# Kernel tuning notes

Hardware: AMD Instinct MI355X
Metric: run time of the kernel (lower is better)

The kernel has to match this reference:

```python
import jax, jax.numpy as jnp
import numpy as np

SEQ, BATCH, IN = 512, 256, 15
H1, H2, FC_HID, NUM_CLASSES = 512, 512, 64, 1


def setup_inputs() -> dict:
    key = jax.random.key(0)
    ks = jax.random.split(key, 14)
    def u(k, shape, fan_in):
        b = 1.0 / np.sqrt(fan_in)
        return jax.random.uniform(k, shape, jnp.float32, -b, b)
    return {
        "x": jax.random.normal(ks[0], (SEQ, BATCH, IN), jnp.float32),
        # PyTorch LSTM params, gate order i,f,g,o stacked along dim 0
        "W_ih1": u(ks[1], (4 * H1, IN), H1),
        "W_hh1": u(ks[2], (4 * H1, H1), H1),
        "b_ih1": u(ks[3], (4 * H1,), H1),
        "b_hh1": u(ks[4], (4 * H1,), H1),
        "W_ih2": u(ks[5], (4 * H2, H1), H2),
        "W_hh2": u(ks[6], (4 * H2, H2), H2),
        "b_ih2": u(ks[7], (4 * H2,), H2),
        "b_hh2": u(ks[8], (4 * H2,), H2),
        "fc1_w": u(ks[9], (FC_HID, H2), H2),
        "fc1_b": u(ks[10], (FC_HID,), H2),
        "fc_w": u(ks[11], (NUM_CLASSES, FC_HID), FC_HID),
        "fc_b": u(ks[12], (NUM_CLASSES,), FC_HID),
    }


def _lstm_cell(x_t, h, c, W_ih, W_hh, b_ih, b_hh):
    # gates: [B, 4H], PyTorch gate order i, f, g, o
    g = x_t @ W_ih.T + b_ih + h @ W_hh.T + b_hh
    i, f, gg, o = jnp.split(g, 4, axis=-1)
    c_new = jax.nn.sigmoid(f) * c + jax.nn.sigmoid(i) * jnp.tanh(gg)
    h_new = jax.nn.sigmoid(o) * jnp.tanh(c_new)
    return h_new, c_new


def reference(x, W_ih1, W_hh1, b_ih1, b_hh1, W_ih2, W_hh2, b_ih2, b_hh2,
              fc1_w, fc1_b, fc_w, fc_b):
    S, B, _ = x.shape
    init = (jnp.zeros((B, H1), x.dtype), jnp.zeros((B, H1), x.dtype),
            jnp.zeros((B, H2), x.dtype), jnp.zeros((B, H2), x.dtype))

    def step(carry, x_t):
        h1, c1, h2, c2 = carry
        h1, c1 = _lstm_cell(x_t, h1, c1, W_ih1, W_hh1, b_ih1, b_hh1)
        h2, c2 = _lstm_cell(h1, h2, c2, W_ih2, W_hh2, b_ih2, b_hh2)
        return (h1, c1, h2, c2), None

    (h1, c1, h2, c2), _ = jax.lax.scan(step, init, x)
    # MLP head on final-timestep top-layer hidden state; `out += out` doubles it
    hn = jax.nn.relu(h2)
    out = jax.nn.relu(hn @ fc1_w.T + fc1_b)
    out = out @ fc_w.T + fc_b
    return out + out
```

## Files before the change

kernel.cpp:

```cpp
#include <hip/hip_runtime.h>
#include <cstdint>
#include <cstddef>

typedef __attribute__((ext_vector_type(8))) short short8;
typedef __attribute__((ext_vector_type(4))) float floatx4;

constexpr int kSeq = 512;
constexpr int kBatch = 256;
constexpr int kIn = 15;
constexpr int kH = 512;
constexpr int kG = 4 * kH;
constexpr int kRing = 17;
constexpr size_t kHSlot = (size_t)kBatch * kH;
constexpr size_t kShmemBytes = 131072 + 4096;

__device__ __forceinline__ unsigned short f2bf(float f) {
    union { float f; unsigned u; } v; v.f = f;
    unsigned u = v.u;
    return (unsigned short)((u + 0x7fffu + ((u >> 16) & 1u)) >> 16);
}

__device__ __forceinline__ float sigm(float x) { return 1.0f / (1.0f + __expf(-x)); }
__device__ __forceinline__ float tanh_(float x) { return 1.0f - 2.0f / (1.0f + __expf(2.0f * x)); }

#define LLC_STORE16(P, V)                                                     \
    asm volatile("global_store_dwordx4 %0, %1, off sc0 sc1"                   \
                 :: "v"(P), "v"(V) : "memory")

__device__ __forceinline__ void waitf(const int* flags, int tgt, int lane, int& fc) {
    if (tgt <= 0) return;
    bool watch = (lane < 32);
    if (__all(!watch || fc >= tgt)) return;
    for (;;) {
        if (watch && fc < tgt)
            fc = __hip_atomic_load(flags + lane * 16,
                                   __ATOMIC_RELAXED, __HIP_MEMORY_SCOPE_AGENT);
        if (__all(!watch || fc >= tgt)) return;
        __builtin_amdgcn_s_sleep(1);
    }
}

__global__ void k_conv(const float* __restrict__ src, unsigned short* __restrict__ dst, int n) {
    int i = blockIdx.x * blockDim.x + threadIdx.x;
    if (i < n) dst[i] = f2bf(src[i]);
}

__global__ void k_conv_pad(const float* __restrict__ src, unsigned short* __restrict__ dst, int rows) {
    int i = blockIdx.x * blockDim.x + threadIdx.x;
    if (i >= rows * 32) return;
    int r = i >> 5, k = i & 31;
    dst[i] = (k < kIn) ? f2bf(src[r * kIn + k]) : (unsigned short)0;
}

__global__ __launch_bounds__(256) void k_persist(
    const unsigned short* __restrict__ whh1b,
    const unsigned short* __restrict__ wih1b,
    const unsigned short* __restrict__ wih2b,
    const unsigned short* __restrict__ whh2b,
    const unsigned short* __restrict__ xb,
    const float* __restrict__ bih1, const float* __restrict__ bhh1,
    const float* __restrict__ bih2, const float* __restrict__ bhh2,
    unsigned short* __restrict__ h1r,
    unsigned short* __restrict__ h2r,
    float* __restrict__ h2f,
    int* __restrict__ flags)
{
    extern __shared__ unsigned short lw[];
    const int bid = blockIdx.x;
    const int g = bid & 3;
    const int role = bid >> 2;
    const bool is2 = role >= 32;
    const int rid = role & 31;
    const int j0 = rid << 4;
    const int tid = (int)threadIdx.x;
    const int wave = tid >> 6;
    const int lane = tid & 63;
    const int lcol = lane & 15;
    const int quad = lane >> 4;
    const int m0 = (g << 6) + wave * 16;
    const int arow = m0 + lcol;
    const int koff = quad * 8;

    int* f1 = flags + g * 1024;
    int* f2 = f1 + 512;
    int* myflag = (is2 ? f2 : f1) + rid * 16;
    unsigned short* scr = lw + 65536 + wave * 384;

    if (!is2) {
        for (int i = tid; i < 4096; i += 256) {
            int ln = i >> 6, gg = ln >> 4, u = ln & 15;
            int c = i & 63, kk = c >> 2, qd = c & 3;
            *(short8*)&lw[((gg * 16 + kk) << 9) + ((qd * 16 + u) << 3)] =
                *(const short8*)&whh1b[(size_t)((gg << 9) + j0 + u) * kH + c * 8];
        }
        for (int i = tid; i < 256; i += 256) {
            int ln = i >> 2, gg = ln >> 4, u = ln & 15;
            int qd = i & 3;
            *(short8*)&lw[((64 + gg) << 9) + ((qd * 16 + u) << 3)] =
                *(const short8*)&wih1b[((gg << 9) + j0 + u) * 32 + qd * 8];
        }
    } else {
        for (int i = tid; i < 4096; i += 256) {
            int ln = i >> 6, gg = ln >> 4, u = ln & 15;
            int c = i & 63, kk = c >> 2, qd = c & 3;
            int dst = ((gg * 16 + kk) << 9) + ((qd * 16 + u) << 3);
            size_t src = (size_t)((gg << 9) + j0 + u) * kH + c * 8;
            *(short8*)&lw[dst] = *(const short8*)&wih2b[src];
            *(short8*)&lw[dst + (64 << 9)] = *(const short8*)&whh2b[src];
        }
    }
    float bsum[4];
#pragma unroll
    for (int gg = 0; gg < 4; ++gg) {
        int n = (gg << 9) + j0 + lcol;
        bsum[gg] = is2 ? (bih2[n] + bhh2[n]) : (bih1[n] + bhh1[n]);
    }
    __syncthreads();

    float creg[4] = {0.f, 0.f, 0.f, 0.f};
    int fc1 = 0, fc2 = 0;

    if (!is2) {
        for (int s = 0; s < kSeq; ++s) {
            if ((s & 15) == 0) {
                if (wave == 0) { waitf(f1, s, lane, fc1); waitf(f2, s, lane, fc2); }
                __syncthreads();
                __builtin_amdgcn_fence(__ATOMIC_ACQUIRE, "agent");
            }
            floatx4 acc[4];
#pragma unroll
            for (int gg = 0; gg < 4; ++gg)
                acc[gg] = (floatx4){bsum[gg], bsum[gg], bsum[gg], bsum[gg]};

            short8 ax = *(const short8*)(xb + ((size_t)s * kBatch + arow) * 32 + koff);

            if (wave == 0) waitf(f1, s, lane, fc1);
            __syncthreads();

            const unsigned short* hp = h1r + (size_t)((s + 16) % kRing) * kHSlot
                                       + (size_t)arow * kH + koff;
            short8 a[16];
#pragma unroll
            for (int kk = 0; kk < 16; ++kk) a[kk] = *(const short8*)(hp + kk * 32);
#pragma unroll
            for (int kk = 0; kk < 16; ++kk) {
#pragma unroll
                for (int gg = 0; gg < 4; ++gg) {
                    short8 b = *(const short8*)&lw[((gg * 16 + kk) << 9) + (lane << 3)];
                    acc[gg] = __builtin_amdgcn_mfma_f32_16x16x32_bf16(a[kk], b, acc[gg], 0, 0, 0);
                }
            }
#pragma unroll
            for (int gg = 0; gg < 4; ++gg) {
                short8 b = *(const short8*)&lw[((64 + gg) << 9) + (lane << 3)];
                acc[gg] = __builtin_amdgcn_mfma_f32_16x16x32_bf16(ax, b, acc[gg], 0, 0, 0);
            }

            unsigned short* hw = h1r + (size_t)(s % kRing) * kHSlot;
#pragma unroll
            for (int r = 0; r < 4; ++r) {
                int row = quad * 4 + r;
                float gi = acc[0][r], gf = acc[1][r], ggv = acc[2][r], go = acc[3][r];
                float cn = sigm(gf) * creg[r] + sigm(gi) * tanh_(ggv);
                float hn = sigm(go) * tanh_(cn);
                creg[r] = cn;
                scr[row * 24 + lcol] = f2bf(hn);
            }
            __syncthreads();
            if (lane < 32) {
                int row = lane >> 1, seg = lane & 1;
                short8 v = *(short8*)&scr[row * 24 + seg * 8];
                unsigned short* gp = hw + (size_t)(m0 + row) * kH + j0 + seg * 8;
                LLC_STORE16(gp, v);
            }
            __builtin_amdgcn_s_waitcnt(0);
            __syncthreads();
            if (tid == 0)
                __hip_atomic_store(myflag, s + 1,
                                   __ATOMIC_RELAXED, __HIP_MEMORY_SCOPE_AGENT);
        }
    } else {
        for (int u = 0; u < kSeq; ++u) {
            if ((u & 15) == 0) {
                if (wave == 0) { waitf(f1, u, lane, fc1); waitf(f2, u, lane, fc2); }
                __syncthreads();
                __builtin_amdgcn_fence(__ATOMIC_ACQUIRE, "agent");
            }
            floatx4 acc[4];
#pragma unroll
            for (int gg = 0; gg < 4; ++gg)
                acc[gg] = (floatx4){bsum[gg], bsum[gg], bsum[gg], bsum[gg]};

            if (wave == 0) waitf(f2, u, lane, fc2);
            __syncthreads();

            const unsigned short* hp2 = h2r + (size_t)((u + 16) % kRing) * kHSlot
                                        + (size_t)arow * kH + koff;
            short8 a[16];
#pragma unroll
            for (int kk = 0; kk < 16; ++kk) a[kk] = *(const short8*)(hp2 + kk * 32);
#pragma unroll
            for (int kk = 0; kk < 16; ++kk) {
#pragma unroll
                for (int gg = 0; gg < 4; ++gg) {
                    short8 b = *(const short8*)&lw[((64 + gg * 16 + kk) << 9) + (lane << 3)];
                    acc[gg] = __builtin_amdgcn_mfma_f32_16x16x32_bf16(a[kk], b, acc[gg], 0, 0, 0);
                }
            }

            if (wave == 0) waitf(f1, u + 1, lane, fc1);
            __syncthreads();

            const unsigned short* hp1 = h1r + (size_t)(u % kRing) * kHSlot
                                        + (size_t)arow * kH + koff;
#pragma unroll
            for (int kk = 0; kk < 16; ++kk) a[kk] = *(const short8*)(hp1 + kk * 32);
#pragma unroll
            for (int kk = 0; kk < 16; ++kk) {
#pragma unroll
                for (int gg = 0; gg < 4; ++gg) {
                    short8 b = *(const short8*)&lw[((gg * 16 + kk) << 9) + (lane << 3)];
                    acc[gg] = __builtin_amdgcn_mfma_f32_16x16x32_bf16(a[kk], b, acc[gg], 0, 0, 0);
                }
            }

            unsigned short* hw = h2r + (size_t)(u % kRing) * kHSlot;
            const int j = j0 + lcol;
#pragma unroll
            for (int r = 0; r < 4; ++r) {
                int row = quad * 4 + r;
                float gi = acc[0][r], gf = acc[1][r], ggv = acc[2][r], go = acc[3][r];
                float cn = sigm(gf) * creg[r] + sigm(gi) * tanh_(ggv);
                float hn = sigm(go) * tanh_(cn);
                creg[r] = cn;
                scr[row * 24 + lcol] = f2bf(hn);
                if (u == kSeq - 1) h2f[(size_t)(m0 + row) * kH + j] = hn;
            }
            __syncthreads();
            if (lane < 32) {
                int row = lane >> 1, seg = lane & 1;
                short8 v = *(short8*)&scr[row * 24 + seg * 8];
                unsigned short* gp = hw + (size_t)(m0 + row) * kH + j0 + seg * 8;
                LLC_STORE16(gp, v);
            }
            __builtin_amdgcn_s_waitcnt(0);
            __syncthreads();
            if (tid == 0)
                __hip_atomic_store(myflag, u + 1,
                                   __ATOMIC_RELAXED, __HIP_MEMORY_SCOPE_AGENT);
        }
    }
}

__global__ __launch_bounds__(64) void k_head(
    const float* __restrict__ h2f, const float* __restrict__ fc1w,
    const float* __restrict__ fc1b, const float* __restrict__ fcw,
    const float* __restrict__ fcb, float* __restrict__ out)
{
    int m = blockIdx.x;
    int j = threadIdx.x;
    const float* hr = h2f + (size_t)m * kH;
    const float* wr = fc1w + (size_t)j * kH;
    float sacc = 0.f;
    for (int k = 0; k < kH; ++k) sacc += fmaxf(hr[k], 0.f) * wr[k];
    float rv = fmaxf(sacc + fc1b[j], 0.f) * fcw[j];
#pragma unroll
    for (int off = 32; off >= 1; off >>= 1) rv += __shfl_down(rv, off);
    if (j == 0) out[m] = 2.0f * (rv + fcb[0]);
}

extern "C" void kernel_launch(void* const* d_in, const int* in_sizes, int n_in,
                              void* d_out, int out_size, void* d_ws, size_t ws_size,
                              hipStream_t stream) {
    const float* x    = (const float*)d_in[0];
    const float* Wih1 = (const float*)d_in[1];
    const float* Whh1 = (const float*)d_in[2];
    const float* bih1 = (const float*)d_in[3];
    const float* bhh1 = (const float*)d_in[4];
    const float* Wih2 = (const float*)d_in[5];
    const float* Whh2 = (const float*)d_in[6];
    const float* bih2 = (const float*)d_in[7];
    const float* bhh2 = (const float*)d_in[8];
    const float* fc1w = (const float*)d_in[9];
    const float* fc1b = (const float*)d_in[10];
    const float* fcw  = (const float*)d_in[11];
    const float* fcb  = (const float*)d_in[12];
    float* out = (float*)d_out;

    char* p = (char*)d_ws;
    auto take = [&](size_t bytes) -> char* {
        char* r = p;
        p += (bytes + 255) & ~(size_t)255;
        return r;
    };
    unsigned short* whh1b = (unsigned short*)take((size_t)kG * kH * 2);
    unsigned short* wih2b = (unsigned short*)take((size_t)kG * kH * 2);
    unsigned short* whh2b = (unsigned short*)take((size_t)kG * kH * 2);
    unsigned short* wih1b = (unsigned short*)take((size_t)kG * 32 * 2);
    unsigned short* xb    = (unsigned short*)take((size_t)kSeq * kBatch * 32 * 2);
    char* state = p;
    unsigned short* h1r = (unsigned short*)take((size_t)kRing * kHSlot * 2);
    unsigned short* h2r = (unsigned short*)take((size_t)kRing * kHSlot * 2);
    int* flags = (int*)take(16384);
    size_t state_bytes = (size_t)((char*)flags + 16384 - state);
    float* h2f = (float*)take((size_t)kBatch * kH * 4);

    hipMemsetAsync(state, 0, state_bytes, stream);

    int n = kG * kH;
    k_conv<<<(n + 255) / 256, 256, 0, stream>>>(Whh1, whh1b, n);
    k_conv<<<(n + 255) / 256, 256, 0, stream>>>(Wih2, wih2b, n);
    k_conv<<<(n + 255) / 256, 256, 0, stream>>>(Whh2, whh2b, n);
    k_conv_pad<<<(kG * 32 + 255) / 256, 256, 0, stream>>>(Wih1, wih1b, kG);
    k_conv_pad<<<(kSeq * kBatch * 32 + 255) / 256, 256, 0, stream>>>(x, xb, kSeq * kBatch);

    hipFuncSetAttribute((const void*)k_persist,
                        hipFuncAttributeMaxDynamicSharedMemorySize, (int)kShmemBytes);
    void* args[] = {&whh1b, &wih1b, &wih2b, &whh2b, &xb,
                    (void*)&bih1, (void*)&bhh1, (void*)&bih2, (void*)&bhh2,
                    &h1r, &h2r, &h2f, &flags};
    hipError_t e = hipLaunchCooperativeKernel((const void*)k_persist, dim3(256), dim3(256),
                                              args, (unsigned)kShmemBytes, stream);
    if (e != hipSuccess) {
        k_persist<<<256, 256, kShmemBytes, stream>>>(
            whh1b, wih1b, wih2b, whh2b, xb, bih1, bhh1, bih2, bhh2,
            h1r, h2r, h2f, flags);
    }

    k_head<<<kBatch, 64, 0, stream>>>(h2f, fc1w, fc1b, fcw, fcb, out);
}
```

Measured before the change: 4.209 ms.

## Switch to per-wave dataflow flags and drop block barriers in persistent LSTM loop

Replaces block-level __syncthreads plus one flag per block with a flag per wave, so each wave waits only on the wave-matched producers covering its batch rows and signals its own progress. The x-projection MFMAs are moved ahead of the wait, and in layer 2 the W_ih·h1 product runs before waiting on h2, to overlap compute with dependency waits. The flag publish is deferred to the next step, after a waitcnt, so stores drain during other work. s_sleep in the spin loop is removed, and the flag array grows fourfold. This adds more polling traffic and relies on per-wave scratch not needing a barrier.

```diff
diff --git a/kernel.cpp b/kernel.cpp
--- a/kernel.cpp
+++ b/kernel.cpp
@@ -36,7 +36,6 @@
             fc = __hip_atomic_load(flags + lane * 16,
                                    __ATOMIC_RELAXED, __HIP_MEMORY_SCOPE_AGENT);
         if (__all(!watch || fc >= tgt)) return;
-        __builtin_amdgcn_s_sleep(1);
     }
 }
 
@@ -81,9 +80,10 @@
     const int arow = m0 + lcol;
     const int koff = quad * 8;
 
-    int* f1 = flags + g * 1024;
-    int* f2 = f1 + 512;
-    int* myflag = (is2 ? f2 : f1) + rid * 16;
+    int* fg = flags + g * 4096;
+    int* f1w = fg + wave * 512;
+    int* f2w = fg + 2048 + wave * 512;
+    int* myflag = (is2 ? f2w : f1w) + rid * 16;
     unsigned short* scr = lw + 65536 + wave * 384;
 
     if (!is2) {
@@ -122,20 +122,29 @@
 
     if (!is2) {
         for (int s = 0; s < kSeq; ++s) {
-            if ((s & 15) == 0) {
-                if (wave == 0) { waitf(f1, s, lane, fc1); waitf(f2, s, lane, fc2); }
-                __syncthreads();
-                __builtin_amdgcn_fence(__ATOMIC_ACQUIRE, "agent");
-            }
             floatx4 acc[4];
 #pragma unroll
             for (int gg = 0; gg < 4; ++gg)
                 acc[gg] = (floatx4){bsum[gg], bsum[gg], bsum[gg], bsum[gg]};
 
             short8 ax = *(const short8*)(xb + ((size_t)s * kBatch + arow) * 32 + koff);
-
-            if (wave == 0) waitf(f1, s, lane, fc1);
-            __syncthreads();
+#pragma unroll
+            for (int gg = 0; gg < 4; ++gg) {
+                short8 b = *(const short8*)&lw[((64 + gg) << 9) + (lane << 3)];
+                acc[gg] = __builtin_amdgcn_mfma_f32_16x16x32_bf16(ax, b, acc[gg], 0, 0, 0);
+            }
+            __builtin_amdgcn_s_waitcnt(0);
+            if ((s & 15) == 0) {
+                if (s > 0 && lane == 0)
+                    __hip_atomic_store(myflag, s, __ATOMIC_RELAXED, __HIP_MEMORY_SCOPE_AGENT);
+                waitf(f1w, s, lane, fc1);
+                waitf(f2w, s, lane, fc2);
+                __builtin_amdgcn_fence(__ATOMIC_ACQUIRE, "agent");
+            } else {
+                if (lane == 0)
+                    __hip_atomic_store(myflag, s, __ATOMIC_RELAXED, __HIP_MEMORY_SCOPE_AGENT);
+                waitf(f1w, s, lane, fc1);
+            }
 
             const unsigned short* hp = h1r + (size_t)((s + 16) % kRing) * kHSlot
                                        + (size_t)arow * kH + koff;
@@ -149,11 +158,6 @@
                     short8 b = *(const short8*)&lw[((gg * 16 + kk) << 9) + (lane << 3)];
                     acc[gg] = __builtin_amdgcn_mfma_f32_16x16x32_bf16(a[kk], b, acc[gg], 0, 0, 0);
                 }
-            }
-#pragma unroll
-            for (int gg = 0; gg < 4; ++gg) {
-                short8 b = *(const short8*)&lw[((64 + gg) << 9) + (lane << 3)];
-                acc[gg] = __builtin_amdgcn_mfma_f32_16x16x32_bf16(ax, b, acc[gg], 0, 0, 0);
             }
 
             unsigned short* hw = h1r + (size_t)(s % kRing) * kHSlot;
@@ -166,37 +170,55 @@
                 creg[r] = cn;
                 scr[row * 24 + lcol] = f2bf(hn);
             }
-            __syncthreads();
             if (lane < 32) {
                 int row = lane >> 1, seg = lane & 1;
                 short8 v = *(short8*)&scr[row * 24 + seg * 8];
                 unsigned short* gp = hw + (size_t)(m0 + row) * kH + j0 + seg * 8;
                 LLC_STORE16(gp, v);
             }
-            __builtin_amdgcn_s_waitcnt(0);
-            __syncthreads();
-            if (tid == 0)
-                __hip_atomic_store(myflag, s + 1,
-                                   __ATOMIC_RELAXED, __HIP_MEMORY_SCOPE_AGENT);
-        }
+        }
+        __builtin_amdgcn_s_waitcnt(0);
+        if (lane == 0)
+            __hip_atomic_store(myflag, kSeq, __ATOMIC_RELAXED, __HIP_MEMORY_SCOPE_AGENT);
     } else {
         for (int u = 0; u < kSeq; ++u) {
-            if ((u & 15) == 0) {
-                if (wave == 0) { waitf(f1, u, lane, fc1); waitf(f2, u, lane, fc2); }
-                __syncthreads();
-                __builtin_amdgcn_fence(__ATOMIC_ACQUIRE, "agent");
-            }
             floatx4 acc[4];
 #pragma unroll
             for (int gg = 0; gg < 4; ++gg)
                 acc[gg] = (floatx4){bsum[gg], bsum[gg], bsum[gg], bsum[gg]};
 
-            if (wave == 0) waitf(f2, u, lane, fc2);
-            __syncthreads();
+            const bool bnd = (u & 15) == 0;
+            if (bnd) {
+                __builtin_amdgcn_s_waitcnt(0);
+                if (u > 0 && lane == 0)
+                    __hip_atomic_store(myflag, u, __ATOMIC_RELAXED, __HIP_MEMORY_SCOPE_AGENT);
+                waitf(f1w, u, lane, fc1);
+                waitf(f2w, u, lane, fc2);
+                __builtin_amdgcn_fence(__ATOMIC_ACQUIRE, "agent");
+            }
+            waitf(f1w, u + 1, lane, fc1);
+
+            const unsigned short* hp1 = h1r + (size_t)(u % kRing) * kHSlot
+                                        + (size_t)arow * kH + koff;
+            short8 a[16];
+#pragma unroll
+            for (int kk = 0; kk < 16; ++kk) a[kk] = *(const short8*)(hp1 + kk * 32);
+#pragma unroll
+            for (int kk = 0; kk < 16; ++kk) {
+#pragma unroll
+                for (int gg = 0; gg < 4; ++gg) {
+                    short8 b = *(const short8*)&lw[((gg * 16 + kk) << 9) + (lane << 3)];
+                    acc[gg] = __builtin_amdgcn_mfma_f32_16x16x32_bf16(a[kk], b, acc[gg], 0, 0, 0);
+                }
+            }
+            __builtin_amdgcn_s_waitcnt(0);
+            if (!bnd && lane == 0)
+                __hip_atomic_store(myflag, u, __ATOMIC_RELAXED, __HIP_MEMORY_SCOPE_AGENT);
+
+            waitf(f2w, u, lane, fc2);
 
             const unsigned short* hp2 = h2r + (size_t)((u + 16) % kRing) * kHSlot
                                         + (size_t)arow * kH + koff;
-            short8 a[16];
 #pragma unroll
             for (int kk = 0; kk < 16; ++kk) a[kk] = *(const short8*)(hp2 + kk * 32);
 #pragma unroll
@@ -204,22 +226,6 @@
 #pragma unroll
                 for (int gg = 0; gg < 4; ++gg) {
                     short8 b = *(const short8*)&lw[((64 + gg * 16 + kk) << 9) + (lane << 3)];
-                    acc[gg] = __builtin_amdgcn_mfma_f32_16x16x32_bf16(a[kk], b, acc[gg], 0, 0, 0);
-                }
-            }
-
-            if (wave == 0) waitf(f1, u + 1, lane, fc1);
-            __syncthreads();
-
-            const unsigned short* hp1 = h1r + (size_t)(u % kRing) * kHSlot
-                                        + (size_t)arow * kH + koff;
-#pragma unroll
-            for (int kk = 0; kk < 16; ++kk) a[kk] = *(const short8*)(hp1 + kk * 32);
-#pragma unroll
-            for (int kk = 0; kk < 16; ++kk) {
-#pragma unroll
-                for (int gg = 0; gg < 4; ++gg) {
-                    short8 b = *(const short8*)&lw[((gg * 16 + kk) << 9) + (lane << 3)];
                     acc[gg] = __builtin_amdgcn_mfma_f32_16x16x32_bf16(a[kk], b, acc[gg], 0, 0, 0);
                 }
             }
@@ -236,18 +242,12 @@
                 scr[row * 24 + lcol] = f2bf(hn);
                 if (u == kSeq - 1) h2f[(size_t)(m0 + row) * kH + j] = hn;
             }
-            __syncthreads();
             if (lane < 32) {
                 int row = lane >> 1, seg = lane & 1;
                 short8 v = *(short8*)&scr[row * 24 + seg * 8];
                 unsigned short* gp = hw + (size_t)(m0 + row) * kH + j0 + seg * 8;
                 LLC_STORE16(gp, v);
             }
-            __builtin_amdgcn_s_waitcnt(0);
-            __syncthreads();
-            if (tid == 0)
-                __hip_atomic_store(myflag, u + 1,
-                                   __ATOMIC_RELAXED, __HIP_MEMORY_SCOPE_AGENT);
         }
     }
 }
@@ -301,8 +301,8 @@
     char* state = p;
     unsigned short* h1r = (unsigned short*)take((size_t)kRing * kHSlot * 2);
     unsigned short* h2r = (unsigned short*)take((size_t)kRing * kHSlot * 2);
-    int* flags = (int*)take(16384);
-    size_t state_bytes = (size_t)((char*)flags + 16384 - state);
+    int* flags = (int*)take(65536);
+    size_t state_bytes = (size_t)((char*)flags + 65536 - state);
     float* h2f = (float*)take((size_t)kBatch * kH * 4);
 
     hipMemsetAsync(state, 0, state_bytes, stream);
```

Measured after the change: 4.699 ms. 11.7% more time.
